# Optimization experiments

Measured on AMD Instinct MI355X. Metric: run time of the kernel, lower is better.

## Reference

```python
import jax, jax.numpy as jnp
import numpy as np
from jax import lax

C = 256  # out_channels
K2 = 1   # a_kernel_size // 2


def _alpha_weights():
    # generate_alpha_weights(dilation=1): (2, 3) constant
    s = float(np.sin(-np.pi / 4.0))
    c = float(np.cos(-np.pi / 4.0))
    aw = np.zeros((2, 3), dtype=np.float32)
    aw[0, 0] = c
    aw[1, 0] = -s
    aw[0, -1] = s
    aw[1, -1] = c
    return jnp.asarray(aw)


def setup_inputs() -> dict:
    key = jax.random.key(0)
    k1, k2, k3 = jax.random.split(key, 3)
    x = jax.random.normal(k1, (32, 256, 64, 64), dtype=jnp.float32)
    w = jax.random.normal(k2, (256, 256, 3, 3), dtype=jnp.float32) * 0.05
    alpha = jax.random.normal(k3, (C, K2, 2, 2), dtype=jnp.float32) * 0.5
    return {"x": x, "w": w, "alpha": alpha}


def _arma_forward(x, w, alpha):
    # moving-average: Conv2d 3x3, stride 1, zero padding 1, no bias
    y = lax.conv_general_dilated(
        x, w, window_strides=(1, 1), padding=[(1, 1), (1, 1)],
        dimension_numbers=("NCHW", "OIHW", "NCHW"))
    B, Co, H, W = y.shape

    aw = _alpha_weights()  # (2, 3)
    at = jnp.tanh(alpha)                       # (C, K2, 2, 2)
    A_xy = jnp.einsum('ckab,bj->ckaj', at, aw)  # (C, K2, 2, 3)
    A_xy = A_xy.at[:, :, :, 1].set(1.0)         # middle tap forced to 1
    A_x = A_xy[:, :, 0:1, :]                    # (C, K2, 1, 3)
    A_y = A_xy[:, :, 1:2, :]                    # (C, K2, 1, 3)
    A = jnp.einsum('ckai,ckbj->ckij', A_x, A_y)  # (C, K2, 3, 3) separable 2D filter
    # pad to (C, K2, H, W) then roll so the center tap sits at the origin
    A_pad = jnp.pad(A, ((0, 0), (0, 0), (0, H - 3), (0, W - 3)))
    A_roll = jnp.roll(A_pad, shift=(-1, -1), axis=(-2, -1))

    # circular AR recursion via frequency-domain division, per dilation chunk
    for k in range(K2):
        a = A_roll[:, k]                        # (C, H, W)
        Yf = jnp.fft.fft2(y) / jnp.fft.fft2(a)  # broadcast (B,C,H,W)/(C,H,W)
        y = jnp.real(jnp.fft.ifft2(Yf))
    return y


def reference(x, w, alpha):
    return _arma_forward(x, w, alpha)
```

## Files before the change

kernel.cpp:

```cpp
#include <hip/hip_runtime.h>
#include <cmath>
#include <stdint.h>

#define HH 64
#define WD 64
#define CIN 256
#define COUT 256
#define NB 32

typedef _Float16 half8 __attribute__((ext_vector_type(8)));
typedef _Float16 half4 __attribute__((ext_vector_type(4)));
typedef float floatx4 __attribute__((ext_vector_type(4)));

#define SB() __builtin_amdgcn_sched_barrier(0)

__device__ __forceinline__ void glds16(const void* src, void* dst) {
    __builtin_amdgcn_global_load_lds((const __attribute__((address_space(1))) void*)src,
                                     (__attribute__((address_space(3))) void*)dst, 16, 0, 0);
}

__global__ __launch_bounds__(256) void xprep_kernel(const float* __restrict__ x,
                                                    _Float16* __restrict__ x16) {
    __shared__ _Float16 lt[32 * 72];
    const int tid = threadIdx.x;
    const int bid = blockIdx.x;
    const int h = bid & 63;
    const int chunk = (bid >> 6) & 7;
    const int n = bid >> 9;
    {
        const int ci = tid >> 3;
        const int w8 = (tid & 7) * 8;
        const float* src = x + (((size_t)(n * 256 + chunk * 32 + ci) * 64 + h) * 64 + w8);
        const float4 a = *(const float4*)src;
        const float4 b = *(const float4*)(src + 4);
        half8 hv;
        hv[0] = (_Float16)a.x; hv[1] = (_Float16)a.y; hv[2] = (_Float16)a.z; hv[3] = (_Float16)a.w;
        hv[4] = (_Float16)b.x; hv[5] = (_Float16)b.y; hv[6] = (_Float16)b.z; hv[7] = (_Float16)b.w;
        *(half8*)&lt[ci * 72 + w8] = hv;
    }
    __syncthreads();
    {
        const int w = tid >> 2;
        const int kc = tid & 3;
        half8 hv;
        #pragma unroll
        for (int j = 0; j < 8; ++j) hv[j] = lt[(kc * 8 + j) * 72 + w];
        *(half8*)&x16[(((size_t)(n * 8 + chunk) * 64 + h) * 64 + w) * 32 + kc * 8] = hv;
    }
}

__global__ __launch_bounds__(256) void wprep_kernel(const float* __restrict__ w,
                                                    _Float16* __restrict__ w16,
                                                    float4* __restrict__ zp) {
    const int idx = blockIdx.x * 256 + threadIdx.x;
    const int j = idx & 7;
    const int m = (idx >> 3) & 15;
    const int q = (idx >> 7) & 3;
    const int u = (idx >> 9) & 3;
    const int rest = idx >> 11;
    const int tap = rest % 9;
    const int rr = rest / 9;
    const int cb = rr & 3;
    const int chunk = rr >> 2;
    const int co = cb * 64 + u * 16 + m;
    const int ci = chunk * 32 + q * 8 + j;
    w16[idx] = (_Float16)w[(co * CIN + ci) * 9 + tap];
    if (blockIdx.x == 0) {
        float4 z; z.x = 0.f; z.y = 0.f; z.z = 0.f; z.w = 0.f;
        zp[threadIdx.x] = z;
    }
}

__global__ __launch_bounds__(256) void gprep1_kernel(const float* __restrict__ alpha,
                                                     float* __restrict__ gtab) {
    const int gid = blockIdx.x * 256 + threadIdx.x;
    const int r   = gid & 63;
    const int isv = (gid >> 6) & 1;
    const int c   = gid >> 7;
    const float t0 = tanhf(alpha[c * 4 + isv * 2 + 0]);
    const float t1 = tanhf(alpha[c * 4 + isv * 2 + 1]);
    const float qq = 0.70710678118654752f;
    const float a0 = qq * (t0 + t1);
    const float a2 = qq * (t1 - t0);
    const float rev = 0.015625f;
    float ssum = 0.f;
    for (int p = 0; p < 64; ++p) {
        const float pr = (float)p * rev;
        const float re = 1.f + (a0 + a2) * __builtin_amdgcn_cosf(pr);
        const float im = (a0 - a2) * __builtin_amdgcn_sinf(pr);
        const float inv = 1.f / (re * re + im * im);
        const float ph = (float)((p * r) & 63) * rev;
        ssum += (__builtin_amdgcn_cosf(ph) * re + __builtin_amdgcn_sinf(ph) * im) * inv;
    }
    gtab[gid] = ssum * (1.0f / 64.0f);
}

__global__ __launch_bounds__(256) void gprep2_kernel(const float* __restrict__ gtab,
                                                     _Float16* __restrict__ gm) {
    const int idx = blockIdx.x * 256 + threadIdx.x;
    const int kc = idx & 7;
    const int row = (idx >> 3) & 63;
    const int which = (idx >> 9) & 1;
    const int c = idx >> 10;
    const float* g = gtab + c * 128 + which * 64;
    half8 hv;
    #pragma unroll
    for (int j = 0; j < 8; ++j)
        hv[j] = (_Float16)g[(row - (kc * 8 + j)) & 63];
    *(half8*)&gm[((size_t)(c * 2 + which) * 64 + row) * 64 + ((kc ^ (row & 7)) * 8)] = hv;
}

__global__ __launch_bounds__(256, 2) void conv_mfma(const _Float16* __restrict__ x16,
                                                    const _Float16* __restrict__ w16,
                                                    const _Float16* __restrict__ zp,
                                                    float* __restrict__ y) {
    extern __shared__ __align__(16) _Float16 xs2[];
    const int tid  = threadIdx.x;
    const int lane = tid & 63;
    const int wv   = tid >> 6;
    const int m    = lane & 15;
    const int q    = lane >> 4;

    const int bid  = blockIdx.x;
    const int xcd  = bid & 7;
    const int idx  = bid >> 3;
    const int sub  = idx & 7;
    const int cb   = sub >> 1;
    const int wt   = sub & 1;
    const int pair = xcd * 16 + (idx >> 3);
    const int ht   = pair & 3;
    const int n    = pair >> 2;
    const int h0   = ht * 16;
    const int w0   = wt * 32;

    int soff[10];
    #pragma unroll
    for (int it = 0; it < 10; ++it) {
        const int slot = it * 256 + tid;
        const int row  = (slot * 7711) >> 20;
        const int rem  = slot - row * 136;
        const int col  = rem >> 2;
        const int oct  = (rem & 3) ^ (col & 3);
        const int gh   = h0 - 1 + row;
        const int gw   = w0 - 1 + col;
        soff[it] = ((unsigned)gh < 64u && (unsigned)gw < 64u)
                 ? ((gh * 64 + gw) * 32 + oct * 8) : -1;
    }

    int aoff[3];
    #pragma unroll
    for (int kx = 0; kx < 3; ++kx)
        aoff[kx] = (m + kx) * 32 + ((q ^ ((m + kx) & 3)) * 8);

    floatx4 acc[4][2][4];
    #pragma unroll
    for (int ro = 0; ro < 4; ++ro)
        #pragma unroll
        for (int cbk = 0; cbk < 2; ++cbk)
            #pragma unroll
            for (int u = 0; u < 4; ++u) acc[ro][cbk][u] = (floatx4)0.f;

    {
        const _Float16* xc0 = x16 + (size_t)n * 1048576;
        #pragma unroll
        for (int it = 0; it < 10; ++it) {
            if (it * 256 + tid < 2448) {
                const _Float16* src = (soff[it] >= 0) ? xc0 + soff[it] : zp + (lane << 3);
                glds16(src, xs2 + (size_t)(it * 256 + wv * 64) * 8);
            }
        }
    }
    asm volatile("s_waitcnt vmcnt(0)" ::: "memory");
    __syncthreads();

    for (int c = 0; c < 8; ++c) {
        _Float16* bcur = xs2 + (c & 1) * 19584;
        _Float16* bnxt = xs2 + ((c & 1) ^ 1) * 19584;
        const _Float16* wchunk = w16 + (size_t)(c * 4 + cb) * 18432;
        const _Float16* xcn = x16 + (size_t)(n * 8 + c + 1) * 131072;
        const bool pf = (c < 7);

        #pragma unroll
        for (int kx = 0; kx < 3; ++kx) {
            half8 bf[3][4];
            #pragma unroll
            for (int ky = 0; ky < 3; ++ky)
                #pragma unroll
                for (int u = 0; u < 4; ++u)
                    bf[ky][u] = *(const half8*)&wchunk[(ky * 3 + kx) * 2048 + u * 512 + lane * 8];

            if (kx == 0 && pf) {
                SB();
                #pragma unroll
                for (int it = 0; it < 5; ++it) {
                    const _Float16* src = (soff[it] >= 0) ? xcn + soff[it] : zp + (lane << 3);
                    glds16(src, bnxt + (size_t)(it * 256 + wv * 64) * 8);
                }
                SB();
            }
            if (kx == 1 && pf) {
                SB();
                #pragma unroll
                for (int it = 5; it < 10; ++it) {
                    if (it * 256 + tid < 2448) {
                        const _Float16* src = (soff[it] >= 0) ? xcn + soff[it] : zp + (lane << 3);
                        glds16(src, bnxt + (size_t)(it * 256 + wv * 64) * 8);
                    }
                }
                SB();
            }

            #pragma unroll
            for (int cbk = 0; cbk < 2; ++cbk) {
                half8 af[6];
                #pragma unroll
                for (int rr = 0; rr < 6; ++rr)
                    af[rr] = *(const half8*)&bcur[(wv * 4 + rr) * 1088 + cbk * 512 + aoff[kx]];
                __builtin_amdgcn_s_setprio(1);
                #pragma unroll
                for (int ro = 0; ro < 4; ++ro)
                    #pragma unroll
                    for (int ky = 0; ky < 3; ++ky)
                        #pragma unroll
                        for (int u = 0; u < 4; ++u)
                            acc[ro][cbk][u] = __builtin_amdgcn_mfma_f32_16x16x32_f16(
                                bf[ky][u], af[ro + ky], acc[ro][cbk][u], 0, 0, 0);
                __builtin_amdgcn_s_setprio(0);
            }
        }
        asm volatile("s_waitcnt vmcnt(0)" ::: "memory");
        __syncthreads();
    }

    _Float16* y16o = (_Float16*)y;
    #pragma unroll
    for (int u = 0; u < 4; ++u) {
        #pragma unroll
        for (int r = 0; r < 4; ++r) {
            const int co = cb * 64 + u * 16 + q * 4 + r;
            _Float16* yp = y16o + (size_t)(n * COUT + co) * 8192 + 4096;
            #pragma unroll
            for (int ro = 0; ro < 4; ++ro)
                #pragma unroll
                for (int cbk = 0; cbk < 2; ++cbk)
                    yp[(h0 + wv * 4 + ro) * 64 + w0 + cbk * 16 + m] = (_Float16)acc[ro][cbk][u][r];
        }
    }
}

__global__ __launch_bounds__(256, 4) void solve_mfma(const _Float16* __restrict__ gm,
                                                     float* __restrict__ y) {
    __shared__ __align__(16) _Float16 Ysd[2][64 * 64];
    __shared__ __align__(16) _Float16 Tt[64 * 64];
    __shared__ __align__(16) _Float16 Gsh[2 * 64 * 64];
    const int tid  = threadIdx.x;
    const int lane = tid & 63;
    const int wv   = tid >> 6;
    const int m    = lane & 15;
    const int q    = lane >> 4;
    const int bid  = blockIdx.x;
    const int nq   = bid & 7;
    const int c    = bid >> 3;

    {
        const _Float16* gsrc = gm + (size_t)c * 8192;
        #pragma unroll
        for (int it = 0; it < 4; ++it)
            glds16(gsrc + (size_t)(it * 256 + tid) * 8, Gsh + (size_t)(it * 256 + wv * 64) * 8);
    }
    {
        const _Float16* ysrc = (const _Float16*)y + ((size_t)(nq * 4 + 0) * 256 + c) * 8192 + 4096;
        #pragma unroll
        for (int it = 0; it < 2; ++it) {
            const int s  = it * 256 + tid;
            const int r  = s >> 3;
            const int kc = (s & 7) ^ (r & 7);
            glds16(ysrc + r * 64 + kc * 8, Ysd[0] + (size_t)(it * 256 + wv * 64) * 8);
        }
    }
    asm volatile("s_waitcnt vmcnt(0)" ::: "memory");
    __syncthreads();

    #pragma unroll
    for (int i = 0; i < 4; ++i) {
        const _Float16* Ys = Ysd[i & 1];
        if (i < 3) {
            const _Float16* ysrc = (const _Float16*)y + ((size_t)(nq * 4 + i + 1) * 256 + c) * 8192 + 4096;
            #pragma unroll
            for (int it = 0; it < 2; ++it) {
                const int s  = it * 256 + tid;
                const int r  = s >> 3;
                const int kc = (s & 7) ^ (r & 7);
                glds16(ysrc + r * 64 + kc * 8, Ysd[(i & 1) ^ 1] + (size_t)(it * 256 + wv * 64) * 8);
            }
        }

        {
            floatx4 acc1[4];
            #pragma unroll
            for (int u = 0; u < 4; ++u) acc1[u] = (floatx4)0.f;
            #pragma unroll
            for (int ks = 0; ks < 2; ++ks) {
                const int swz = ((ks * 4 + q) ^ (m & 7)) * 8;
                const half8 yf = *(const half8*)&Ys[(16 * wv + m) * 64 + swz];
                #pragma unroll
                for (int u = 0; u < 4; ++u) {
                    const half8 gvf = *(const half8*)&Gsh[4096 + (u * 16 + m) * 64 + swz];
                    acc1[u] = __builtin_amdgcn_mfma_f32_16x16x32_f16(yf, gvf, acc1[u], 0, 0, 0);
                }
            }
            #pragma unroll
            for (int u = 0; u < 4; ++u) {
                half4 hv;
                #pragma unroll
                for (int r = 0; r < 4; ++r) hv[r] = (_Float16)acc1[u][r];
                const int s = u * 16 + m;
                const int kc = 2 * wv + (q >> 1);
                *(half4*)&Tt[s * 64 + ((kc ^ (s & 7)) * 8) + (q & 1) * 4] = hv;
            }
        }
        __syncthreads();

        {
            float* yp = y + ((size_t)(nq * 4 + i) * 256 + c) * 4096;
            floatx4 acc2[4];
            #pragma unroll
            for (int u = 0; u < 4; ++u) acc2[u] = (floatx4)0.f;
            #pragma unroll
            for (int ks = 0; ks < 2; ++ks) {
                const int swz = ((ks * 4 + q) ^ (m & 7)) * 8;
                const half8 guf = *(const half8*)&Gsh[(16 * wv + m) * 64 + swz];
                #pragma unroll
                for (int u = 0; u < 4; ++u) {
                    const half8 ttf = *(const half8*)&Tt[(u * 16 + m) * 64 + swz];
                    acc2[u] = __builtin_amdgcn_mfma_f32_16x16x32_f16(guf, ttf, acc2[u], 0, 0, 0);
                }
            }
            #pragma unroll
            for (int u = 0; u < 4; ++u)
                #pragma unroll
                for (int r = 0; r < 4; ++r)
                    yp[(16 * wv + q * 4 + r) * 64 + u * 16 + m] = acc2[u][r];
        }
        if (i < 3) {
            asm volatile("s_waitcnt vmcnt(0)" ::: "memory");
            __syncthreads();
        }
    }
}

extern "C" void kernel_launch(void* const* d_in, const int* in_sizes, int n_in,
                              void* d_out, int out_size, void* d_ws, size_t ws_size,
                              hipStream_t stream) {
    const float* x     = (const float*)d_in[0];
    const float* w     = (const float*)d_in[1];
    const float* alpha = (const float*)d_in[2];
    float* y = (float*)d_out;

    _Float16* x16 = (_Float16*)d_ws;
    _Float16* w16 = (_Float16*)((char*)d_ws + 67108864);
    _Float16* gm  = (_Float16*)((char*)d_ws + 68288512);
    float*    gtab = (float*)((char*)d_ws + 72482816);
    float4*   zp   = (float4*)((char*)d_ws + 72613888);

    static bool inited = false;
    if (!inited) {
        hipFuncSetAttribute((const void*)conv_mfma,
                            hipFuncAttributeMaxDynamicSharedMemorySize, 78336);
        inited = true;
    }

    xprep_kernel <<<dim3(32 * 8 * 64), 256, 0, stream>>>(x, x16);
    wprep_kernel <<<dim3(2304),        256, 0, stream>>>(w, w16, zp);
    gprep1_kernel<<<dim3(128),         256, 0, stream>>>(alpha, gtab);
    gprep2_kernel<<<dim3(1024),        256, 0, stream>>>(gtab, gm);
    conv_mfma    <<<dim3(1024),        256, 78336, stream>>>(x16, w16, (const _Float16*)zp, y);
    solve_mfma   <<<dim3(2048),        256, 0, stream>>>(gm, y);
}
```

Before: 390.4 us.

## Switch conv to 32x32x16 MFMA with matching weight and LDS layouts

Replaces the 16x16x32 f16 MFMA tiles in the implicit-GEMM convolution with 32x32x16 MFMA. The weight prep layout and the LDS input-tile layout change to fit the new operand shapes: 32 output channels per block tile and a split of K into two halves, with the XOR swizzle replaced by a padded row stride of 34. The aim is fewer MFMA instructions and fewer LDS operand reads per unit of work. In exchange, the padded layout may bring back LDS bank conflicts, and accumulator register use and store patterns change.

```diff
diff --git a/kernel.cpp b/kernel.cpp
--- a/kernel.cpp
+++ b/kernel.cpp
@@ -11,6 +11,7 @@
 typedef _Float16 half8 __attribute__((ext_vector_type(8)));
 typedef _Float16 half4 __attribute__((ext_vector_type(4)));
 typedef float floatx4 __attribute__((ext_vector_type(4)));
+typedef float floatx16 __attribute__((ext_vector_type(16)));
 
 #define SB() __builtin_amdgcn_sched_barrier(0)
 
@@ -53,17 +54,17 @@
                                                     _Float16* __restrict__ w16,
                                                     float4* __restrict__ zp) {
     const int idx = blockIdx.x * 256 + threadIdx.x;
-    const int j = idx & 7;
-    const int m = (idx >> 3) & 15;
-    const int q = (idx >> 7) & 3;
-    const int u = (idx >> 9) & 3;
-    const int rest = idx >> 11;
-    const int tap = rest % 9;
-    const int rr = rest / 9;
-    const int cb = rr & 3;
+    const int j    = idx & 7;
+    const int lane = (idx >> 3) & 63;
+    const int cob  = (idx >> 9) & 1;
+    const int ks   = (idx >> 10) & 1;
+    const int t2   = idx >> 11;
+    const int tap  = t2 % 9;
+    const int rr   = t2 / 9;
+    const int cb   = rr & 3;
     const int chunk = rr >> 2;
-    const int co = cb * 64 + u * 16 + m;
-    const int ci = chunk * 32 + q * 8 + j;
+    const int co = cb * 64 + cob * 32 + (lane & 31);
+    const int ci = chunk * 32 + ks * 16 + (lane >> 5) * 8 + j;
     w16[idx] = (_Float16)w[(co * CIN + ci) * 9 + tap];
     if (blockIdx.x == 0) {
         float4 z; z.x = 0.f; z.y = 0.f; z.z = 0.f; z.w = 0.f;
@@ -118,8 +119,8 @@
     const int tid  = threadIdx.x;
     const int lane = tid & 63;
     const int wv   = tid >> 6;
-    const int m    = lane & 15;
-    const int q    = lane >> 4;
+    const int l31  = lane & 31;
+    const int kh   = lane >> 5;
 
     const int bid  = blockIdx.x;
     const int xcd  = bid & 7;
@@ -139,26 +140,21 @@
         const int slot = it * 256 + tid;
         const int row  = (slot * 7711) >> 20;
         const int rem  = slot - row * 136;
-        const int col  = rem >> 2;
-        const int oct  = (rem & 3) ^ (col & 3);
+        const int oct  = (rem * 241) >> 13;
+        const int col  = rem - oct * 34;
         const int gh   = h0 - 1 + row;
         const int gw   = w0 - 1 + col;
         soff[it] = ((unsigned)gh < 64u && (unsigned)gw < 64u)
                  ? ((gh * 64 + gw) * 32 + oct * 8) : -1;
     }
 
-    int aoff[3];
-    #pragma unroll
-    for (int kx = 0; kx < 3; ++kx)
-        aoff[kx] = (m + kx) * 32 + ((q ^ ((m + kx) & 3)) * 8);
-
-    floatx4 acc[4][2][4];
+    const int albase = (kh * 34 + l31) * 8;
+
+    floatx16 acc[4][2];
     #pragma unroll
     for (int ro = 0; ro < 4; ++ro)
         #pragma unroll
-        for (int cbk = 0; cbk < 2; ++cbk)
-            #pragma unroll
-            for (int u = 0; u < 4; ++u) acc[ro][cbk][u] = (floatx4)0.f;
+        for (int cob = 0; cob < 2; ++cob) acc[ro][cob] = (floatx16)0.f;
 
     {
         const _Float16* xc0 = x16 + (size_t)n * 1048576;
@@ -182,12 +178,15 @@
 
         #pragma unroll
         for (int kx = 0; kx < 3; ++kx) {
-            half8 bf[3][4];
-            #pragma unroll
-            for (int ky = 0; ky < 3; ++ky)
-                #pragma unroll
-                for (int u = 0; u < 4; ++u)
-                    bf[ky][u] = *(const half8*)&wchunk[(ky * 3 + kx) * 2048 + u * 512 + lane * 8];
+            half8 bf[2][3][2];
+            #pragma unroll
+            for (int ks = 0; ks < 2; ++ks)
+                #pragma unroll
+                for (int ky = 0; ky < 3; ++ky)
+                    #pragma unroll
+                    for (int cob = 0; cob < 2; ++cob)
+                        bf[ks][ky][cob] = *(const half8*)&wchunk[
+                            ((ky * 3 + kx) * 4 + ks * 2 + cob) * 512 + lane * 8];
 
             if (kx == 0 && pf) {
                 SB();
@@ -211,20 +210,21 @@
             }
 
             #pragma unroll
-            for (int cbk = 0; cbk < 2; ++cbk) {
+            for (int ks = 0; ks < 2; ++ks) {
                 half8 af[6];
                 #pragma unroll
                 for (int rr = 0; rr < 6; ++rr)
-                    af[rr] = *(const half8*)&bcur[(wv * 4 + rr) * 1088 + cbk * 512 + aoff[kx]];
+                    af[rr] = *(const half8*)&bcur[
+                        ((wv * 4 + rr) * 136 + ks * 68 + kx) * 8 + albase];
                 __builtin_amdgcn_s_setprio(1);
                 #pragma unroll
-                for (int ro = 0; ro < 4; ++ro)
+                for (int ky = 0; ky < 3; ++ky)
                     #pragma unroll
-                    for (int ky = 0; ky < 3; ++ky)
+                    for (int ro = 0; ro < 4; ++ro)
                         #pragma unroll
-                        for (int u = 0; u < 4; ++u)
-                            acc[ro][cbk][u] = __builtin_amdgcn_mfma_f32_16x16x32_f16(
-                                bf[ky][u], af[ro + ky], acc[ro][cbk][u], 0, 0, 0);
+                        for (int cob = 0; cob < 2; ++cob)
+                            acc[ro][cob] = __builtin_amdgcn_mfma_f32_32x32x16_f16(
+                                bf[ks][ky][cob], af[ro + ky], acc[ro][cob], 0, 0, 0);
                 __builtin_amdgcn_s_setprio(0);
             }
         }
@@ -234,16 +234,14 @@
 
     _Float16* y16o = (_Float16*)y;
     #pragma unroll
-    for (int u = 0; u < 4; ++u) {
-        #pragma unroll
-        for (int r = 0; r < 4; ++r) {
-            const int co = cb * 64 + u * 16 + q * 4 + r;
+    for (int cob = 0; cob < 2; ++cob) {
+        #pragma unroll
+        for (int reg = 0; reg < 16; ++reg) {
+            const int co = cb * 64 + cob * 32 + (reg & 3) + 8 * (reg >> 2) + 4 * kh;
             _Float16* yp = y16o + (size_t)(n * COUT + co) * 8192 + 4096;
             #pragma unroll
             for (int ro = 0; ro < 4; ++ro)
-                #pragma unroll
-                for (int cbk = 0; cbk < 2; ++cbk)
-                    yp[(h0 + wv * 4 + ro) * 64 + w0 + cbk * 16 + m] = (_Float16)acc[ro][cbk][u][r];
+                yp[(h0 + wv * 4 + ro) * 64 + w0 + l31] = (_Float16)acc[ro][cob][reg];
         }
     }
 }
```

Measured after the change: 421.4 us. +7.9%, slower.

## Fuse gprep kernels and restructure solve to per-wave 32x32 MFMA images

Applied to the files above, without the earlier changes.

The two filter-table prep kernels are merged into one launch that keeps the intermediate table in shared memory. solve_mfma is reorganised so each wave handles a whole 64x64 image with 32x32x16 MFMAs. Each wave loads its Y operands straight from global into registers and keeps a private transpose buffer, which removes the block-wide barriers and the LDS double-buffering of Y. The trade-off is more LDS per block (occupancy bound lowered to 3) and uncoalesced per-lane global fragment loads. The blockIdx is also remapped across XCDs.

```diff
diff --git a/kernel.cpp b/kernel.cpp
--- a/kernel.cpp
+++ b/kernel.cpp
@@ -11,6 +11,7 @@
 typedef _Float16 half8 __attribute__((ext_vector_type(8)));
 typedef _Float16 half4 __attribute__((ext_vector_type(4)));
 typedef float floatx4 __attribute__((ext_vector_type(4)));
+typedef float floatx16 __attribute__((ext_vector_type(16)));
 
 #define SB() __builtin_amdgcn_sched_barrier(0)
 
@@ -71,43 +72,45 @@
     }
 }
 
-__global__ __launch_bounds__(256) void gprep1_kernel(const float* __restrict__ alpha,
-                                                     float* __restrict__ gtab) {
-    const int gid = blockIdx.x * 256 + threadIdx.x;
-    const int r   = gid & 63;
-    const int isv = (gid >> 6) & 1;
-    const int c   = gid >> 7;
-    const float t0 = tanhf(alpha[c * 4 + isv * 2 + 0]);
-    const float t1 = tanhf(alpha[c * 4 + isv * 2 + 1]);
-    const float qq = 0.70710678118654752f;
-    const float a0 = qq * (t0 + t1);
-    const float a2 = qq * (t1 - t0);
-    const float rev = 0.015625f;
-    float ssum = 0.f;
-    for (int p = 0; p < 64; ++p) {
-        const float pr = (float)p * rev;
-        const float re = 1.f + (a0 + a2) * __builtin_amdgcn_cosf(pr);
-        const float im = (a0 - a2) * __builtin_amdgcn_sinf(pr);
-        const float inv = 1.f / (re * re + im * im);
-        const float ph = (float)((p * r) & 63) * rev;
-        ssum += (__builtin_amdgcn_cosf(ph) * re + __builtin_amdgcn_sinf(ph) * im) * inv;
-    }
-    gtab[gid] = ssum * (1.0f / 64.0f);
-}
-
-__global__ __launch_bounds__(256) void gprep2_kernel(const float* __restrict__ gtab,
-                                                     _Float16* __restrict__ gm) {
-    const int idx = blockIdx.x * 256 + threadIdx.x;
-    const int kc = idx & 7;
-    const int row = (idx >> 3) & 63;
-    const int which = (idx >> 9) & 1;
-    const int c = idx >> 10;
-    const float* g = gtab + c * 128 + which * 64;
-    half8 hv;
-    #pragma unroll
-    for (int j = 0; j < 8; ++j)
-        hv[j] = (_Float16)g[(row - (kc * 8 + j)) & 63];
-    *(half8*)&gm[((size_t)(c * 2 + which) * 64 + row) * 64 + ((kc ^ (row & 7)) * 8)] = hv;
+__global__ __launch_bounds__(256) void gprep_kernel(const float* __restrict__ alpha,
+                                                    _Float16* __restrict__ gm) {
+    __shared__ float gl[128];
+    const int c = blockIdx.x;
+    const int tid = threadIdx.x;
+    if (tid < 128) {
+        const int r   = tid & 63;
+        const int isv = tid >> 6;
+        const float t0 = tanhf(alpha[c * 4 + isv * 2 + 0]);
+        const float t1 = tanhf(alpha[c * 4 + isv * 2 + 1]);
+        const float qq = 0.70710678118654752f;
+        const float a0 = qq * (t0 + t1);
+        const float a2 = qq * (t1 - t0);
+        const float rev = 0.015625f;
+        float ssum = 0.f;
+        for (int p = 0; p < 64; ++p) {
+            const float pr = (float)p * rev;
+            const float re = 1.f + (a0 + a2) * __builtin_amdgcn_cosf(pr);
+            const float im = (a0 - a2) * __builtin_amdgcn_sinf(pr);
+            const float inv = 1.f / (re * re + im * im);
+            const float ph = (float)((p * r) & 63) * rev;
+            ssum += (__builtin_amdgcn_cosf(ph) * re + __builtin_amdgcn_sinf(ph) * im) * inv;
+        }
+        gl[tid] = ssum * (1.0f / 64.0f);
+    }
+    __syncthreads();
+    #pragma unroll
+    for (int it = 0; it < 4; ++it) {
+        const int idx = it * 256 + tid;
+        const int kc = idx & 7;
+        const int row = (idx >> 3) & 63;
+        const int which = idx >> 9;
+        const float* g = gl + which * 64;
+        half8 hv;
+        #pragma unroll
+        for (int j = 0; j < 8; ++j)
+            hv[j] = (_Float16)g[(row - (kc * 8 + j)) & 63];
+        *(half8*)&gm[((size_t)(c * 2 + which) * 64 + row) * 64 + ((kc ^ (row & 7)) * 8)] = hv;
+    }
 }
 
 __global__ __launch_bounds__(256, 2) void conv_mfma(const _Float16* __restrict__ x16,
@@ -248,19 +251,21 @@
     }
 }
 
-__global__ __launch_bounds__(256, 4) void solve_mfma(const _Float16* __restrict__ gm,
+__global__ __launch_bounds__(256, 3) void solve_mfma(const _Float16* __restrict__ gm,
                                                      float* __restrict__ y) {
-    __shared__ __align__(16) _Float16 Ysd[2][64 * 64];
-    __shared__ __align__(16) _Float16 Tt[64 * 64];
     __shared__ __align__(16) _Float16 Gsh[2 * 64 * 64];
+    __shared__ __align__(16) _Float16 TT[4][64 * 64];
     const int tid  = threadIdx.x;
     const int lane = tid & 63;
     const int wv   = tid >> 6;
-    const int m    = lane & 15;
-    const int q    = lane >> 4;
-    const int bid  = blockIdx.x;
-    const int nq   = bid & 7;
-    const int c    = bid >> 3;
+    const int l31  = lane & 31;
+    const int kh   = lane >> 5;
+
+    const int bid = blockIdx.x;
+    const int wg  = (bid & 7) * 256 + (bid >> 3);
+    const int c   = wg >> 3;
+    const int nq  = wg & 7;
+    const int n   = nq * 4 + wv;
 
     {
         const _Float16* gsrc = gm + (size_t)c * 8192;
@@ -268,85 +273,97 @@
         for (int it = 0; it < 4; ++it)
             glds16(gsrc + (size_t)(it * 256 + tid) * 8, Gsh + (size_t)(it * 256 + wv * 64) * 8);
     }
-    {
-        const _Float16* ysrc = (const _Float16*)y + ((size_t)(nq * 4 + 0) * 256 + c) * 8192 + 4096;
-        #pragma unroll
-        for (int it = 0; it < 2; ++it) {
-            const int s  = it * 256 + tid;
-            const int r  = s >> 3;
-            const int kc = (s & 7) ^ (r & 7);
-            glds16(ysrc + r * 64 + kc * 8, Ysd[0] + (size_t)(it * 256 + wv * 64) * 8);
-        }
-    }
     asm volatile("s_waitcnt vmcnt(0)" ::: "memory");
     __syncthreads();
 
-    #pragma unroll
-    for (int i = 0; i < 4; ++i) {
-        const _Float16* Ys = Ysd[i & 1];
-        if (i < 3) {
-            const _Float16* ysrc = (const _Float16*)y + ((size_t)(nq * 4 + i + 1) * 256 + c) * 8192 + 4096;
-            #pragma unroll
-            for (int it = 0; it < 2; ++it) {
-                const int s  = it * 256 + tid;
-                const int r  = s >> 3;
-                const int kc = (s & 7) ^ (r & 7);
-                glds16(ysrc + r * 64 + kc * 8, Ysd[(i & 1) ^ 1] + (size_t)(it * 256 + wv * 64) * 8);
-            }
-        }
-
-        {
-            floatx4 acc1[4];
-            #pragma unroll
-            for (int u = 0; u < 4; ++u) acc1[u] = (floatx4)0.f;
-            #pragma unroll
-            for (int ks = 0; ks < 2; ++ks) {
-                const int swz = ((ks * 4 + q) ^ (m & 7)) * 8;
-                const half8 yf = *(const half8*)&Ys[(16 * wv + m) * 64 + swz];
-                #pragma unroll
-                for (int u = 0; u < 4; ++u) {
-                    const half8 gvf = *(const half8*)&Gsh[4096 + (u * 16 + m) * 64 + swz];
-                    acc1[u] = __builtin_amdgcn_mfma_f32_16x16x32_f16(yf, gvf, acc1[u], 0, 0, 0);
-                }
-            }
-            #pragma unroll
-            for (int u = 0; u < 4; ++u) {
+    const _Float16* ysrc = (const _Float16*)y + ((size_t)n * 256 + c) * 8192 + 4096;
+    float* yp = y + ((size_t)n * 256 + c) * 4096;
+    _Float16* tt = TT[wv];
+
+    floatx16 a1[2][2];
+    #pragma unroll
+    for (int tr = 0; tr < 2; ++tr)
+        #pragma unroll
+        for (int tc = 0; tc < 2; ++tc) a1[tr][tc] = (floatx16)0.f;
+
+    half8 yf[2][4];
+    #pragma unroll
+    for (int tr = 0; tr < 2; ++tr)
+        #pragma unroll
+        for (int ks = 0; ks < 4; ++ks)
+            yf[tr][ks] = *(const half8*)&ysrc[(32 * tr + l31) * 64 + ks * 16 + kh * 8];
+
+    #pragma unroll
+    for (int ks = 0; ks < 4; ++ks) {
+        const int kc = ks * 2 + kh;
+        half8 gv[2];
+        #pragma unroll
+        for (int tc = 0; tc < 2; ++tc) {
+            const int row = 32 * tc + l31;
+            gv[tc] = *(const half8*)&Gsh[4096 + row * 64 + ((kc ^ (row & 7)) * 8)];
+        }
+        #pragma unroll
+        for (int tr = 0; tr < 2; ++tr)
+            #pragma unroll
+            for (int tc = 0; tc < 2; ++tc)
+                a1[tr][tc] = __builtin_amdgcn_mfma_f32_32x32x16_f16(
+                    yf[tr][ks], gv[tc], a1[tr][tc], 0, 0, 0);
+    }
+
+    #pragma unroll
+    for (int tr = 0; tr < 2; ++tr) {
+        #pragma unroll
+        for (int tc = 0; tc < 2; ++tc) {
+            const int tcol = 32 * tc + l31;
+            #pragma unroll
+            for (int q2 = 0; q2 < 4; ++q2) {
                 half4 hv;
                 #pragma unroll
-                for (int r = 0; r < 4; ++r) hv[r] = (_Float16)acc1[u][r];
-                const int s = u * 16 + m;
-                const int kc = 2 * wv + (q >> 1);
-                *(half4*)&Tt[s * 64 + ((kc ^ (s & 7)) * 8) + (q & 1) * 4] = hv;
-            }
-        }
-        __syncthreads();
-
-        {
-            float* yp = y + ((size_t)(nq * 4 + i) * 256 + c) * 4096;
-            floatx4 acc2[4];
-            #pragma unroll
-            for (int u = 0; u < 4; ++u) acc2[u] = (floatx4)0.f;
-            #pragma unroll
-            for (int ks = 0; ks < 2; ++ks) {
-                const int swz = ((ks * 4 + q) ^ (m & 7)) * 8;
-                const half8 guf = *(const half8*)&Gsh[(16 * wv + m) * 64 + swz];
-                #pragma unroll
-                for (int u = 0; u < 4; ++u) {
-                    const half8 ttf = *(const half8*)&Tt[(u * 16 + m) * 64 + swz];
-                    acc2[u] = __builtin_amdgcn_mfma_f32_16x16x32_f16(guf, ttf, acc2[u], 0, 0, 0);
-                }
-            }
-            #pragma unroll
-            for (int u = 0; u < 4; ++u)
-                #pragma unroll
-                for (int r = 0; r < 4; ++r)
-                    yp[(16 * wv + q * 4 + r) * 64 + u * 16 + m] = acc2[u][r];
-        }
-        if (i < 3) {
-            asm volatile("s_waitcnt vmcnt(0)" ::: "memory");
-            __syncthreads();
-        }
-    }
+                for (int rq = 0; rq < 4; ++rq) hv[rq] = (_Float16)a1[tr][tc][q2 * 4 + rq];
+                *(half4*)&tt[tcol * 64 + (((4 * tr + q2) ^ (tcol & 7)) * 8) + 4 * kh] = hv;
+            }
+        }
+    }
+    asm volatile("s_waitcnt lgkmcnt(0)" ::: "memory");
+    __builtin_amdgcn_sched_barrier(0);
+
+    floatx16 a2[2][2];
+    #pragma unroll
+    for (int tr = 0; tr < 2; ++tr)
+        #pragma unroll
+        for (int tc = 0; tc < 2; ++tc) a2[tr][tc] = (floatx16)0.f;
+
+    #pragma unroll
+    for (int ks = 0; ks < 4; ++ks) {
+        const int kc = ks * 2 + kh;
+        half8 gu[2], tb[2];
+        #pragma unroll
+        for (int tr = 0; tr < 2; ++tr) {
+            const int row = 32 * tr + l31;
+            gu[tr] = *(const half8*)&Gsh[row * 64 + ((kc ^ (row & 7)) * 8)];
+        }
+        #pragma unroll
+        for (int tc = 0; tc < 2; ++tc) {
+            const int col = 32 * tc + l31;
+            tb[tc] = *(const half8*)&tt[col * 64 + ((kc ^ (col & 7)) * 8)];
+        }
+        #pragma unroll
+        for (int tr = 0; tr < 2; ++tr)
+            #pragma unroll
+            for (int tc = 0; tc < 2; ++tc)
+                a2[tr][tc] = __builtin_amdgcn_mfma_f32_32x32x16_f16(
+                    gu[tr], tb[tc], a2[tr][tc], 0, 0, 0);
+    }
+
+    #pragma unroll
+    for (int tr = 0; tr < 2; ++tr)
+        #pragma unroll
+        for (int tc = 0; tc < 2; ++tc)
+            #pragma unroll
+            for (int reg = 0; reg < 16; ++reg) {
+                const int row = 32 * tr + (reg & 3) + 8 * (reg >> 2) + 4 * kh;
+                yp[row * 64 + 32 * tc + l31] = a2[tr][tc][reg];
+            }
 }
 
 extern "C" void kernel_launch(void* const* d_in, const int* in_sizes, int n_in,
@@ -360,7 +377,6 @@
     _Float16* x16 = (_Float16*)d_ws;
     _Float16* w16 = (_Float16*)((char*)d_ws + 67108864);
     _Float16* gm  = (_Float16*)((char*)d_ws + 68288512);
-    float*    gtab = (float*)((char*)d_ws + 72482816);
     float4*   zp   = (float4*)((char*)d_ws + 72613888);
 
     static bool inited = false;
@@ -372,8 +388,7 @@
 
     xprep_kernel <<<dim3(32 * 8 * 64), 256, 0, stream>>>(x, x16);
     wprep_kernel <<<dim3(2304),        256, 0, stream>>>(w, w16, zp);
-    gprep1_kernel<<<dim3(128),         256, 0, stream>>>(alpha, gtab);
-    gprep2_kernel<<<dim3(1024),        256, 0, stream>>>(gtab, gm);
+    gprep_kernel <<<dim3(256),         256, 0, stream>>>(alpha, gm);
     conv_mfma    <<<dim3(1024),        256, 78336, stream>>>(x16, w16, (const _Float16*)zp, y);
     solve_mfma   <<<dim3(2048),        256, 0, stream>>>(gm, y);
 }
```

Result: faster. 381.0 us (-2.4%).
